# Kernel tuning notes

Hardware: AMD Instinct MI355X
Metric: run time of the kernel (lower is better)

The kernel has to match this reference:

```python
import jax, jax.numpy as jnp
import numpy as np

DIM, HID, E, K = 512, 2048, 8, 2

def setup_inputs() -> dict:
    key = jax.random.key(0)
    ks = jax.random.split(key, 6)
    x = jax.random.normal(ks[0], (8, 4096, DIM), dtype=jnp.float32)
    assign = jax.random.randint(ks[1], (8, 4096, K), 0, E, dtype=jnp.int32)
    W1 = jax.random.normal(ks[2], (E, DIM, HID), dtype=jnp.float32) * 0.02
    b1 = jnp.zeros((E, HID), dtype=jnp.float32)
    W2 = jax.random.normal(ks[3], (E, HID, DIM), dtype=jnp.float32) * 0.02
    b2 = jnp.zeros((E, DIM), dtype=jnp.float32)
    return {"x": x, "assign": assign, "W1": W1, "b1": b1, "W2": W2, "b2": b2}

def reference(x, assign, W1, b1, W2, b2):
    # x: [B,S,D]; assign: [B,S,K] expert ids; hash router => uniform weights 1/K
    B, S, D = x.shape
    k = assign.shape[-1]
    num_experts = W1.shape[0]
    flat_x = x.reshape(B * S, D)
    flat_assign = assign.reshape(B * S, k)
    inv_k = jnp.asarray(1.0 / k, dtype=x.dtype)
    out = jnp.zeros((B * S, D), dtype=x.dtype)
    for e in range(num_experts):  # small fixed expert count
        # total routing weight for this expert per token (handles duplicate slots)
        token_w = (flat_assign == e).sum(-1).astype(x.dtype) * inv_k  # [B*S]
        h = jax.nn.relu(flat_x @ W1[e] + b1[e])        # [B*S, hidden]
        y = h @ W2[e] + b2[e]                          # [B*S, D]
        out = out + y * token_w[:, None]               # zero weight => zero contribution
    return out.reshape(B, S, D)
```

## Files before the change

### kernel.cpp

```cpp
#include <hip/hip_runtime.h>


#define NTOK 32768
#define DIM  512
#define HID  2048
#define NE   8
#define TM   64
#define MAXTILE 128

#define XBASE 0
#define HBASE 65536
#define RBASE 98304
#define LDS_BYTES 163840

typedef __attribute__((ext_vector_type(8))) short short8;
typedef __attribute__((ext_vector_type(4))) float f32x4;
typedef __attribute__((ext_vector_type(4))) unsigned short us4b;
typedef unsigned short ushort_t;

__device__ __forceinline__ unsigned short f2bf(float f) {
  union { float f; unsigned u; } v; v.f = f;
  unsigned r = v.u + 0x7FFFu + ((v.u >> 16) & 1u);
  return (unsigned short)(r >> 16);
}
__device__ __forceinline__ float bf2f(unsigned short s) {
  union { unsigned u; float f; } v; v.u = ((unsigned)s) << 16;
  return v.f;
}
__device__ __forceinline__ void g2l16(const void* g, void* l) {
  __builtin_amdgcn_global_load_lds(
      (const __attribute__((address_space(1))) void*)g,
      (__attribute__((address_space(3))) void*)l, 16, 0, 0);
}

#define SCHB __builtin_amdgcn_sched_barrier(0)
#define VMW4 do { asm volatile("s_waitcnt vmcnt(4)" ::: "memory"); SCHB; } while (0)
#define MFMA16(a, b, c) __builtin_amdgcn_mfma_f32_16x16x32_bf16(a, b, c, 0, 0, 0)

__device__ __forceinline__ void transp_body(const float* __restrict__ src,
                                            ushort_t* __restrict__ dst,
                                            int R, int C, int rb, int cb,
                                            int t, float tile[64][68]) {
  {
    const int tr = t >> 2, tc = (t & 3) * 16;
    const f32x4* s = (const f32x4*)(src + (size_t)(rb + tr) * C + cb + tc);
    f32x4 v0 = __builtin_nontemporal_load(s + 0);
    f32x4 v1 = __builtin_nontemporal_load(s + 1);
    f32x4 v2 = __builtin_nontemporal_load(s + 2);
    f32x4 v3 = __builtin_nontemporal_load(s + 3);
    *(f32x4*)&tile[tr][tc + 0]  = v0;
    *(f32x4*)&tile[tr][tc + 4]  = v1;
    *(f32x4*)&tile[tr][tc + 8]  = v2;
    *(f32x4*)&tile[tr][tc + 12] = v3;
  }
  __syncthreads();
  {
    const int n = t >> 2, ks = (t & 3) * 16;
    short8 o0, o1;
#pragma unroll
    for (int j = 0; j < 8; ++j) o0[j] = (short)f2bf(tile[ks + j][n]);
#pragma unroll
    for (int j = 0; j < 8; ++j) o1[j] = (short)f2bf(tile[ks + 8 + j][n]);
    ushort_t* d = dst + (size_t)(cb + n) * R + rb + ks;
    *(short8*)(d) = o0;
    *(short8*)(d + 8) = o1;
  }
}

__global__ __launch_bounds__(256) void moe_prep(
    const float* __restrict__ W1, const float* __restrict__ W2,
    ushort_t* __restrict__ W1b, ushort_t* __restrict__ W2b,
    const int* __restrict__ assign, int* __restrict__ cnt,
    int* __restrict__ lists) {
  __shared__ float tile[64][68];
  __shared__ int lcnt[NE], gbase[NE];
  const int b = blockIdx.x;
  const int t = threadIdx.x;
  if (b < 2048) {
    int e = b >> 8, rem = b & 255;
    int rb = (rem >> 5) * 64, cb = (rem & 31) * 64;
    transp_body(W1 + (size_t)e * DIM * HID, W1b + (size_t)e * HID * DIM,
                DIM, HID, rb, cb, t, tile);
  } else if (b < 4096) {
    int bb = b - 2048;
    int e = bb >> 8, rem = bb & 255;
    int rb = (rem >> 3) * 64, cb = (rem & 7) * 64;
    transp_body(W2 + (size_t)e * HID * DIM, W2b + (size_t)e * DIM * HID,
                HID, DIM, rb, cb, t, tile);
  } else {
    int tt = (b - 4096) * 256 + t;
    if (t < NE) lcnt[t] = 0;
    __syncthreads();
    int a0 = assign[2 * tt + 0];
    int a1 = assign[2 * tt + 1];
    int r0, r1 = -1;
    r0 = atomicAdd(&lcnt[a0], 1);
    if (a0 != a1) r1 = atomicAdd(&lcnt[a1], 1);
    __syncthreads();
    if (t < NE) gbase[t] = atomicAdd(&cnt[t], lcnt[t]);
    __syncthreads();
    if (a0 == a1) {
      lists[a0 * NTOK + gbase[a0] + r0] = tt | 0x10000;
    } else {
      lists[a0 * NTOK + gbase[a0] + r0] = tt;
      lists[a1 * NTOK + gbase[a1] + r1] = tt | (1 << 17);
    }
  }
}

__global__ __launch_bounds__(256) void moe_combine(
    const ushort_t* __restrict__ Yb, float* __restrict__ out) {
  size_t i = ((size_t)blockIdx.x * 256 + threadIdx.x) * 8;
  short8 y0 = *(const short8*)(Yb + i);
  short8 y1 = *(const short8*)(Yb + (size_t)NTOK * DIM + i);
  f32x4 o0, o1;
#pragma unroll
  for (int j = 0; j < 4; ++j)
    o0[j] = 0.5f * (bf2f((unsigned short)y0[j]) + bf2f((unsigned short)y1[j]));
#pragma unroll
  for (int j = 0; j < 4; ++j)
    o1[j] = 0.5f * (bf2f((unsigned short)y0[4 + j]) + bf2f((unsigned short)y1[4 + j]));
  *(f32x4*)(out + i) = o0;
  *(f32x4*)(out + i + 4) = o1;
}

__global__ __launch_bounds__(512, 1) void moe_gemm(
    const float* __restrict__ x, const ushort_t* __restrict__ W1b,
    const float* __restrict__ b1, const ushort_t* __restrict__ W2b,
    const float* __restrict__ b2, const int* __restrict__ cnt,
    const int* __restrict__ lists, ushort_t* __restrict__ Yb) {
  extern __shared__ char smem[];

  const int id = blockIdx.x;
  const int e = id & 7;
  const int tile = id >> 3;
  const int n_e = cnt[e];
  const int t0 = tile * TM;
  if (t0 >= n_e) return;

  const int tid = threadIdx.x;
  const int wid = tid >> 6;
  const int lane = tid & 63;
  const int lr = lane & 15, lg = lane >> 4;
  const int lr7 = lr & 7;
  const int lrq = (lr >> 1) & 3;
  const int l3 = lane >> 3, l7 = lane & 7;

  char* const ring0 = smem + RBASE + wid * 8192;

  const ushort_t* gW1c = W1b + ((size_t)(e * HID) + wid * 32 + l3) * DIM + (l7 ^ l3) * 8;
  const ushort_t* gW2c = W2b + ((size_t)(e * DIM) + wid * 64 + (lane >> 2)) * HID +
                         ((lane & 3) ^ ((lane >> 3) & 3)) * 8;
  const float* b1e = b1 + (size_t)e * HID + wid * 32 + lg * 4;

  auto IS_G1 = [&](const ushort_t* wb, int p, int half, int slot) {
    char* d = ring0 + slot * 2048 + lane * 16;
    const ushort_t* g = wb + (size_t)(half * 16) * DIM + p * 64;
    g2l16(g, d);
    g2l16(g + (size_t)8 * DIM, d + 1024);
  };
  auto IS_G2 = [&](const ushort_t* wb, int q, int h, int slot) {
    char* d = ring0 + slot * 2048 + lane * 16;
    const ushort_t* g = wb + (size_t)(h * 32) * HID + q * 32;
    g2l16(g, d);
    g2l16(g + (size_t)16 * HID, d + 1024);
  };

#define B1LOAD(d0, d1, BI) do { \
  const float* a_ = b1e + (BI) * 256; \
  asm volatile("global_load_dwordx4 %0, %2, off\n\t" \
               "global_load_dwordx4 %1, %2, off offset:64" \
               : "=&v"(d0), "=&v"(d1) : "v"(a_)); \
} while (0)

#define XRD(dst, nf, p, kf) do { \
  const int row_ = (nf) * 16 + lr; \
  const int u_ = (p) * 8 + (kf) * 4 + lg; \
  dst = *(const short8*)(smem + XBASE + row_ * 1024 + \
        ((u_ & ~7) | ((u_ & 7) ^ (row_ & 7))) * 16); } while (0)
#define HRD(dst, nf, q) do { \
  const int row_ = (nf) * 16 + lr; \
  const int u_ = (q) * 4 + lg; \
  dst = *(const short8*)(smem + HBASE + row_ * 512 + \
        ((u_ & ~7) | ((u_ & 7) ^ (row_ & 7))) * 16); } while (0)
#define W1RD(dst, S, kf) \
  dst = *(const short8*)(ring0 + (S) * 2048 + lr * 128 + ((((kf) * 4 + lg) ^ lr7) * 16))
#define W2RD(dst, S, half) \
  dst = *(const short8*)(ring0 + (S) * 2048 + ((half) * 16 + lr) * 64 + ((lg ^ lrq) * 16))

#define G1_PHASE(p, S0, S1, ISS) do { \
  VMW4; \
  short8 wa0k0, wa1k0, wa0k1, wa1k1; \
  W1RD(wa0k0, S0, 0); W1RD(wa1k0, S1, 0); W1RD(wa0k1, S0, 1); W1RD(wa1k1, S1, 1); \
  SCHB; \
  short8 x00, x01, x02, x03, x10, x11, x12, x13; \
  XRD(x00, 0, p, 0); XRD(x01, 1, p, 0); XRD(x02, 2, p, 0); XRD(x03, 3, p, 0); \
  XRD(x10, 0, p, 1); XRD(x11, 1, p, 1); XRD(x12, 2, p, 1); XRD(x13, 3, p, 1); \
  SCHB; \
  asm volatile("s_waitcnt lgkmcnt(8)" ::: "memory"); SCHB; \
  ISS; SCHB; \
  __builtin_amdgcn_s_setprio(1); \
  acc1[0][0] = MFMA16(wa0k0, x00, acc1[0][0]); acc1[1][0] = MFMA16(wa1k0, x00, acc1[1][0]); \
  acc1[0][1] = MFMA16(wa0k0, x01, acc1[0][1]); acc1[1][1] = MFMA16(wa1k0, x01, acc1[1][1]); \
  acc1[0][2] = MFMA16(wa0k0, x02, acc1[0][2]); acc1[1][2] = MFMA16(wa1k0, x02, acc1[1][2]); \
  acc1[0][3] = MFMA16(wa0k0, x03, acc1[0][3]); acc1[1][3] = MFMA16(wa1k0, x03, acc1[1][3]); \
  acc1[0][0] = MFMA16(wa0k1, x10, acc1[0][0]); acc1[1][0] = MFMA16(wa1k1, x10, acc1[1][0]); \
  acc1[0][1] = MFMA16(wa0k1, x11, acc1[0][1]); acc1[1][1] = MFMA16(wa1k1, x11, acc1[1][1]); \
  acc1[0][2] = MFMA16(wa0k1, x12, acc1[0][2]); acc1[1][2] = MFMA16(wa1k1, x12, acc1[1][2]); \
  acc1[0][3] = MFMA16(wa0k1, x13, acc1[0][3]); acc1[1][3] = MFMA16(wa1k1, x13, acc1[1][3]); \
  __builtin_amdgcn_s_setprio(0); SCHB; \
} while (0)

#define G2_PHASE(q, S0, S1, ISS) do { \
  VMW4; \
  short8 w0, w1, w2, w3; \
  W2RD(w0, S0, 0); W2RD(w1, S0, 1); W2RD(w2, S1, 0); W2RD(w3, S1, 1); \
  SCHB; \
  short8 h0, h1, h2, h3; \
  HRD(h0, 0, q); HRD(h1, 1, q); HRD(h2, 2, q); HRD(h3, 3, q); \
  SCHB; \
  asm volatile("s_waitcnt lgkmcnt(4)" ::: "memory"); SCHB; \
  ISS; SCHB; \
  __builtin_amdgcn_s_setprio(1); \
  acc2[0][0] = MFMA16(w0, h0, acc2[0][0]); acc2[0][1] = MFMA16(w0, h1, acc2[0][1]); \
  acc2[0][2] = MFMA16(w0, h2, acc2[0][2]); acc2[0][3] = MFMA16(w0, h3, acc2[0][3]); \
  acc2[1][0] = MFMA16(w1, h0, acc2[1][0]); acc2[1][1] = MFMA16(w1, h1, acc2[1][1]); \
  acc2[1][2] = MFMA16(w1, h2, acc2[1][2]); acc2[1][3] = MFMA16(w1, h3, acc2[1][3]); \
  acc2[2][0] = MFMA16(w2, h0, acc2[2][0]); acc2[2][1] = MFMA16(w2, h1, acc2[2][1]); \
  acc2[2][2] = MFMA16(w2, h2, acc2[2][2]); acc2[2][3] = MFMA16(w2, h3, acc2[2][3]); \
  acc2[3][0] = MFMA16(w3, h0, acc2[3][0]); acc2[3][1] = MFMA16(w3, h1, acc2[3][1]); \
  acc2[3][2] = MFMA16(w3, h2, acc2[3][2]); acc2[3][3] = MFMA16(w3, h3, acc2[3][3]); \
  __builtin_amdgcn_s_setprio(0); SCHB; \
} while (0)

#define HWRITE(Q0, Q1) do { \
  _Pragma("unroll") \
  for (int mf_ = 0; mf_ < 2; ++mf_) { \
    f32x4 bq_ = mf_ ? (Q1) : (Q0); \
    int hl_ = wid * 32 + mf_ * 16 + lg * 4; \
    int u_ = hl_ >> 3; \
    _Pragma("unroll") \
    for (int nf_ = 0; nf_ < 4; ++nf_) { \
      int tokr_ = nf_ * 16 + lr; \
      us4b pk_; \
      pk_.x = f2bf(fmaxf(acc1[mf_][nf_][0] + bq_[0], 0.0f)); \
      pk_.y = f2bf(fmaxf(acc1[mf_][nf_][1] + bq_[1], 0.0f)); \
      pk_.z = f2bf(fmaxf(acc1[mf_][nf_][2] + bq_[2], 0.0f)); \
      pk_.w = f2bf(fmaxf(acc1[mf_][nf_][3] + bq_[3], 0.0f)); \
      int u2_ = (u_ & ~7) | ((u_ & 7) ^ (tokr_ & 7)); \
      *(us4b*)(smem + HBASE + tokr_ * 512 + u2_ * 16 + (lg & 1) * 8) = pk_; \
    } \
  } \
} while (0)

#define CHUNK(C, BU0, BU1, BN0, BN1) do { \
  f32x4 acc1[2][4]; \
  _Pragma("unroll") \
  for (int i_ = 0; i_ < 2; ++i_) \
    _Pragma("unroll") \
    for (int j_ = 0; j_ < 4; ++j_) acc1[i_][j_] = f32x4{0.f, 0.f, 0.f, 0.f}; \
  G1_PHASE(0, 0, 1, { B1LOAD(BN0, BN1, ((C) < 7 ? (C) + 1 : 7)); \
                      IS_G1(gW1c, 2, 0, 0); IS_G1(gW1c, 2, 1, 1); }); \
  G1_PHASE(1, 2, 3, { IS_G1(gW1c, 3, 0, 2); IS_G1(gW1c, 3, 1, 3); }); \
  G1_PHASE(2, 0, 1, { IS_G1(gW1c, 4, 0, 0); IS_G1(gW1c, 4, 1, 1); }); \
  G1_PHASE(3, 2, 3, { IS_G1(gW1c, 5, 0, 2); IS_G1(gW1c, 5, 1, 3); }); \
  G1_PHASE(4, 0, 1, { IS_G1(gW1c, 6, 0, 0); IS_G1(gW1c, 6, 1, 1); }); \
  G1_PHASE(5, 2, 3, { IS_G1(gW1c, 7, 0, 2); IS_G1(gW1c, 7, 1, 3); }); \
  G1_PHASE(6, 0, 1, { IS_G2(gW2c, 0, 0, 0); IS_G2(gW2c, 0, 1, 1); }); \
  G1_PHASE(7, 2, 3, { IS_G2(gW2c, 1, 0, 2); IS_G2(gW2c, 1, 1, 3); }); \
  asm volatile("s_waitcnt lgkmcnt(0)" ::: "memory"); \
  __builtin_amdgcn_s_barrier(); SCHB; \
  HWRITE(BU0, BU1); \
  SCHB; \
  asm volatile("s_waitcnt lgkmcnt(0)" ::: "memory"); \
  __builtin_amdgcn_s_barrier(); SCHB; \
  G2_PHASE(0, 0, 1, { IS_G2(gW2c, 2, 0, 0); IS_G2(gW2c, 2, 1, 1); }); \
  G2_PHASE(1, 2, 3, { IS_G2(gW2c, 3, 0, 2); IS_G2(gW2c, 3, 1, 3); }); \
  G2_PHASE(2, 0, 1, { IS_G2(gW2c, 4, 0, 0); IS_G2(gW2c, 4, 1, 1); }); \
  G2_PHASE(3, 2, 3, { IS_G2(gW2c, 5, 0, 2); IS_G2(gW2c, 5, 1, 3); }); \
  G2_PHASE(4, 0, 1, { IS_G2(gW2c, 6, 0, 0); IS_G2(gW2c, 6, 1, 1); }); \
  G2_PHASE(5, 2, 3, { IS_G2(gW2c, 7, 0, 2); IS_G2(gW2c, 7, 1, 3); }); \
  G2_PHASE(6, 0, 1, { IS_G1(gW1c + 131072, 0, 0, 0); IS_G1(gW1c + 131072, 0, 1, 1); }); \
  G2_PHASE(7, 2, 3, { IS_G1(gW1c + 131072, 1, 0, 2); IS_G1(gW1c + 131072, 1, 1, 3); }); \
  gW1c += 131072; gW2c += 256; \
} while (0)

  {
    int row = tid >> 3;
    int idx = t0 + row;
    int tok = lists[e * NTOK + (idx < n_e ? idx : 0)] & 0xFFFF;
    const float* xr = x + (size_t)tok * DIM;
#pragma unroll
    for (int i = 0; i < 8; ++i) {
      int u = (tid & 7) + 8 * i;
      f32x4 v0 = __builtin_nontemporal_load((const f32x4*)(xr + u * 8));
      f32x4 v1 = __builtin_nontemporal_load((const f32x4*)(xr + u * 8 + 4));
      short8 pk;
      pk[0] = (short)f2bf(v0.x); pk[1] = (short)f2bf(v0.y);
      pk[2] = (short)f2bf(v0.z); pk[3] = (short)f2bf(v0.w);
      pk[4] = (short)f2bf(v1.x); pk[5] = (short)f2bf(v1.y);
      pk[6] = (short)f2bf(v1.z); pk[7] = (short)f2bf(v1.w);
      int su = (u & ~7) | ((u & 7) ^ (row & 7));
      *(short8*)(smem + XBASE + row * 1024 + su * 16) = pk;
    }
  }
  __syncthreads();

  f32x4 b1A0, b1A1, b1B0, b1B1;
  B1LOAD(b1A0, b1A1, 0);
  IS_G1(gW1c, 0, 0, 0); IS_G1(gW1c, 0, 1, 1);
  IS_G1(gW1c, 1, 0, 2); IS_G1(gW1c, 1, 1, 3);
  SCHB;

  f32x4 acc2[4][4];
#pragma unroll
  for (int i = 0; i < 4; ++i)
#pragma unroll
    for (int j = 0; j < 4; ++j) acc2[i][j] = f32x4{0.f, 0.f, 0.f, 0.f};

#pragma unroll 1
  for (int cc = 0; cc < 4; ++cc) {
    const int c0 = cc * 2;
    CHUNK(c0,     b1A0, b1A1, b1B0, b1B1);
    CHUNK(c0 + 1, b1B0, b1B1, b1A0, b1A1);
  }
  asm volatile("s_waitcnt vmcnt(0)" ::: "memory");
  SCHB;
  asm volatile("" :: "v"(b1A0), "v"(b1A1));

  f32x4 b2q[4];
#pragma unroll
  for (int mf = 0; mf < 4; ++mf)
    b2q[mf] = *(const f32x4*)(b2 + e * DIM + wid * 64 + mf * 16 + lg * 4);

#pragma unroll
  for (int nf = 0; nf < 4; ++nf) {
    int gi = t0 + nf * 16 + lr;
    if (gi >= n_e) continue;
    int ent = lists[e * NTOK + gi];
    int tok = ent & 0xFFFF;
    int slot = (ent >> 17) & 1;
    size_t base = ((size_t)(slot * NTOK + tok)) * DIM + wid * 64 + lg * 4;
#pragma unroll
    for (int mf = 0; mf < 4; ++mf) {
      f32x4 y = acc2[mf][nf] + b2q[mf];
      us4b pk;
      pk.x = f2bf(y[0]); pk.y = f2bf(y[1]); pk.z = f2bf(y[2]); pk.w = f2bf(y[3]);
      *(us4b*)(Yb + base + mf * 16) = pk;
      if (ent & 0x10000)
        *(us4b*)(Yb + base + (size_t)NTOK * DIM + mf * 16) = pk;
    }
  }
}

extern "C" void kernel_launch(void* const* d_in, const int* in_sizes, int n_in,
                              void* d_out, int out_size, void* d_ws, size_t ws_size,
                              hipStream_t stream) {
  const float* x      = (const float*)d_in[0];
  const int*   assign = (const int*)d_in[1];
  const float* W1     = (const float*)d_in[2];
  const float* b1     = (const float*)d_in[3];
  const float* W2     = (const float*)d_in[4];
  const float* b2     = (const float*)d_in[5];
  float* out = (float*)d_out;

  char* ws = (char*)d_ws;
  int* cnt   = (int*)ws;
  int* lists = (int*)(ws + 1024);
  ushort_t* W1b = (ushort_t*)(ws + (2ull << 20));
  ushort_t* W2b = (ushort_t*)(ws + (2ull << 20) + 18874368ull);
  ushort_t* Yb  = (ushort_t*)(ws + (2ull << 20) + 2ull * 18874368ull);

  (void)hipMemsetAsync(cnt, 0, 256, stream);

  moe_prep<<<4096 + NTOK / 256, 256, 0, stream>>>(W1, W2, W1b, W2b,
                                                  assign, cnt, lists);

  (void)hipFuncSetAttribute((const void*)moe_gemm,
                            hipFuncAttributeMaxDynamicSharedMemorySize, LDS_BYTES);
  moe_gemm<<<NE * MAXTILE, 512, LDS_BYTES, stream>>>(x, W1b, b1, W2b, b2,
                                                     cnt, lists, Yb);

  moe_combine<<<NTOK * DIM / 2048, 256, 0, stream>>>(Yb, out);
}
```

Baseline: 355.4 us.

## Restructure fused MoE FFN into 512-wide hidden chunks with 64-row weight tiles

Replaces the eight 256-hidden chunks with four 512-hidden chunks. Each wave now computes a 64x64 GEMM1 tile (acc1 grows to 4x4) and stages four 8-row weight groups per slot in a two-slot ring of 4KB slots. In exchange, the H buffer is handed off twice per chunk, each with its own barrier and bias load. The intent is more MFMA per LDS weight read and fewer loop iterations, at the cost of higher register pressure from the larger accumulators and extra handoff barriers.

```diff
diff --git a/kernel.cpp b/kernel.cpp
--- a/kernel.cpp
+++ b/kernel.cpp
@@ -143,146 +143,91 @@
   const int lane = tid & 63;
   const int lr = lane & 15, lg = lane >> 4;
   const int lr7 = lr & 7;
-  const int lrq = (lr >> 1) & 3;
-  const int l3 = lane >> 3, l7 = lane & 7;
-
-  char* const ring0 = smem + RBASE + wid * 8192;
-
-  const ushort_t* gW1c = W1b + ((size_t)(e * HID) + wid * 32 + l3) * DIM + (l7 ^ l3) * 8;
-  const ushort_t* gW2c = W2b + ((size_t)(e * DIM) + wid * 64 + (lane >> 2)) * HID +
-                         ((lane & 3) ^ ((lane >> 3) & 3)) * 8;
-  const float* b1e = b1 + (size_t)e * HID + wid * 32 + lg * 4;
-
-  auto IS_G1 = [&](const ushort_t* wb, int p, int half, int slot) {
-    char* d = ring0 + slot * 2048 + lane * 16;
-    const ushort_t* g = wb + (size_t)(half * 16) * DIM + p * 64;
+  const int lsub = lane >> 3;
+  const int unit = (lane & 7) ^ lsub;
+  const int etahi = unit >> 2;
+  const int kq = unit & 3;
+
+  char* const ringw = smem + RBASE + wid * 8192;
+
+  const ushort_t* gW1w = W1b +
+      ((size_t)(e * HID + wid * 32 + etahi * 256 + lsub)) * DIM + kq * 8;
+  const ushort_t* gW2w = W2b +
+      ((size_t)(e * DIM + wid * 64 + etahi * 32 + lsub)) * HID + kq * 8;
+
+  auto stW1 = [&](int c, int p, int sl) {
+    const ushort_t* g = gW1w + (size_t)c * (512 * DIM) + p * 32;
+    char* d = ringw + sl * 4096 + lane * 16;
     g2l16(g, d);
-    g2l16(g + (size_t)8 * DIM, d + 1024);
+    g2l16(g + 1 * 8 * DIM, d + 1024);
+    g2l16(g + 2 * 8 * DIM, d + 2048);
+    g2l16(g + 3 * 8 * DIM, d + 3072);
   };
-  auto IS_G2 = [&](const ushort_t* wb, int q, int h, int slot) {
-    char* d = ring0 + slot * 2048 + lane * 16;
-    const ushort_t* g = wb + (size_t)(h * 32) * HID + q * 32;
+  auto stW2 = [&](int c, int h, int q, int sl) {
+    const ushort_t* g = gW2w + c * 512 + h * 256 + q * 32;
+    char* d = ringw + sl * 4096 + lane * 16;
     g2l16(g, d);
-    g2l16(g + (size_t)16 * HID, d + 1024);
+    g2l16(g + 1 * 8 * HID, d + 1024);
+    g2l16(g + 2 * 8 * HID, d + 2048);
+    g2l16(g + 3 * 8 * HID, d + 3072);
   };
 
-#define B1LOAD(d0, d1, BI) do { \
-  const float* a_ = b1e + (BI) * 256; \
-  asm volatile("global_load_dwordx4 %0, %2, off\n\t" \
-               "global_load_dwordx4 %1, %2, off offset:64" \
-               : "=&v"(d0), "=&v"(d1) : "v"(a_)); \
-} while (0)
-
-#define XRD(dst, nf, p, kf) do { \
-  const int row_ = (nf) * 16 + lr; \
-  const int u_ = (p) * 8 + (kf) * 4 + lg; \
-  dst = *(const short8*)(smem + XBASE + row_ * 1024 + \
-        ((u_ & ~7) | ((u_ & 7) ^ (row_ & 7))) * 16); } while (0)
-#define HRD(dst, nf, q) do { \
-  const int row_ = (nf) * 16 + lr; \
-  const int u_ = (q) * 4 + lg; \
-  dst = *(const short8*)(smem + HBASE + row_ * 512 + \
-        ((u_ & ~7) | ((u_ & 7) ^ (row_ & 7))) * 16); } while (0)
-#define W1RD(dst, S, kf) \
-  dst = *(const short8*)(ring0 + (S) * 2048 + lr * 128 + ((((kf) * 4 + lg) ^ lr7) * 16))
-#define W2RD(dst, S, half) \
-  dst = *(const short8*)(ring0 + (S) * 2048 + ((half) * 16 + lr) * 64 + ((lg ^ lrq) * 16))
-
-#define G1_PHASE(p, S0, S1, ISS) do { \
-  VMW4; \
-  short8 wa0k0, wa1k0, wa0k1, wa1k1; \
-  W1RD(wa0k0, S0, 0); W1RD(wa1k0, S1, 0); W1RD(wa0k1, S0, 1); W1RD(wa1k1, S1, 1); \
-  SCHB; \
-  short8 x00, x01, x02, x03, x10, x11, x12, x13; \
-  XRD(x00, 0, p, 0); XRD(x01, 1, p, 0); XRD(x02, 2, p, 0); XRD(x03, 3, p, 0); \
-  XRD(x10, 0, p, 1); XRD(x11, 1, p, 1); XRD(x12, 2, p, 1); XRD(x13, 3, p, 1); \
-  SCHB; \
-  asm volatile("s_waitcnt lgkmcnt(8)" ::: "memory"); SCHB; \
-  ISS; SCHB; \
-  __builtin_amdgcn_s_setprio(1); \
-  acc1[0][0] = MFMA16(wa0k0, x00, acc1[0][0]); acc1[1][0] = MFMA16(wa1k0, x00, acc1[1][0]); \
-  acc1[0][1] = MFMA16(wa0k0, x01, acc1[0][1]); acc1[1][1] = MFMA16(wa1k0, x01, acc1[1][1]); \
-  acc1[0][2] = MFMA16(wa0k0, x02, acc1[0][2]); acc1[1][2] = MFMA16(wa1k0, x02, acc1[1][2]); \
-  acc1[0][3] = MFMA16(wa0k0, x03, acc1[0][3]); acc1[1][3] = MFMA16(wa1k0, x03, acc1[1][3]); \
-  acc1[0][0] = MFMA16(wa0k1, x10, acc1[0][0]); acc1[1][0] = MFMA16(wa1k1, x10, acc1[1][0]); \
-  acc1[0][1] = MFMA16(wa0k1, x11, acc1[0][1]); acc1[1][1] = MFMA16(wa1k1, x11, acc1[1][1]); \
-  acc1[0][2] = MFMA16(wa0k1, x12, acc1[0][2]); acc1[1][2] = MFMA16(wa1k1, x12, acc1[1][2]); \
-  acc1[0][3] = MFMA16(wa0k1, x13, acc1[0][3]); acc1[1][3] = MFMA16(wa1k1, x13, acc1[1][3]); \
+#define RD_W(dst, mf, SL) \
+  dst = *(const short8*)(ringw + (SL) * 4096 + (((mf) & 1) * 16 + lr) * 128 + \
+                         (((((mf) >> 1) * 4 + lg) ^ lr7) * 16))
+
+#define G1P(p, SL, ISSUE) do { \
+  ISSUE; SCHB; VMW4; \
+  short8 wf[4], xf[4]; \
+  _Pragma("unroll") for (int mf = 0; mf < 4; ++mf) RD_W(wf[mf], mf, SL); \
+  _Pragma("unroll") for (int nf = 0; nf < 4; ++nf) { \
+    int u_ = (p) * 4 + lg; int row_ = nf * 16 + lr; \
+    xf[nf] = *(const short8*)(smem + XBASE + row_ * 1024 + \
+             ((u_ & ~7) | ((u_ & 7) ^ lr7)) * 16); } \
+  SCHB; __builtin_amdgcn_s_setprio(1); \
+  _Pragma("unroll") for (int mf = 0; mf < 4; ++mf) \
+    _Pragma("unroll") for (int nf = 0; nf < 4; ++nf) \
+      acc1[mf][nf] = MFMA16(wf[mf], xf[nf], acc1[mf][nf]); \
   __builtin_amdgcn_s_setprio(0); SCHB; \
 } while (0)
 
-#define G2_PHASE(q, S0, S1, ISS) do { \
-  VMW4; \
-  short8 w0, w1, w2, w3; \
-  W2RD(w0, S0, 0); W2RD(w1, S0, 1); W2RD(w2, S1, 0); W2RD(w3, S1, 1); \
-  SCHB; \
-  short8 h0, h1, h2, h3; \
-  HRD(h0, 0, q); HRD(h1, 1, q); HRD(h2, 2, q); HRD(h3, 3, q); \
-  SCHB; \
-  asm volatile("s_waitcnt lgkmcnt(4)" ::: "memory"); SCHB; \
-  ISS; SCHB; \
-  __builtin_amdgcn_s_setprio(1); \
-  acc2[0][0] = MFMA16(w0, h0, acc2[0][0]); acc2[0][1] = MFMA16(w0, h1, acc2[0][1]); \
-  acc2[0][2] = MFMA16(w0, h2, acc2[0][2]); acc2[0][3] = MFMA16(w0, h3, acc2[0][3]); \
-  acc2[1][0] = MFMA16(w1, h0, acc2[1][0]); acc2[1][1] = MFMA16(w1, h1, acc2[1][1]); \
-  acc2[1][2] = MFMA16(w1, h2, acc2[1][2]); acc2[1][3] = MFMA16(w1, h3, acc2[1][3]); \
-  acc2[2][0] = MFMA16(w2, h0, acc2[2][0]); acc2[2][1] = MFMA16(w2, h1, acc2[2][1]); \
-  acc2[2][2] = MFMA16(w2, h2, acc2[2][2]); acc2[2][3] = MFMA16(w2, h3, acc2[2][3]); \
-  acc2[3][0] = MFMA16(w3, h0, acc2[3][0]); acc2[3][1] = MFMA16(w3, h1, acc2[3][1]); \
-  acc2[3][2] = MFMA16(w3, h2, acc2[3][2]); acc2[3][3] = MFMA16(w3, h3, acc2[3][3]); \
+#define G2P(q, SL, ISSUE) do { \
+  ISSUE; SCHB; VMW4; \
+  short8 wf[4], hf[4]; \
+  _Pragma("unroll") for (int mf = 0; mf < 4; ++mf) RD_W(wf[mf], mf, SL); \
+  _Pragma("unroll") for (int nf = 0; nf < 4; ++nf) { \
+    int u_ = (q) * 4 + lg; int row_ = nf * 16 + lr; \
+    hf[nf] = *(const short8*)(smem + HBASE + row_ * 512 + \
+             ((u_ & ~7) | ((u_ & 7) ^ lr7)) * 16); } \
+  SCHB; __builtin_amdgcn_s_setprio(1); \
+  _Pragma("unroll") for (int mf = 0; mf < 4; ++mf) \
+    _Pragma("unroll") for (int nf = 0; nf < 4; ++nf) \
+      acc2[mf][nf] = MFMA16(wf[mf], hf[nf], acc2[mf][nf]); \
   __builtin_amdgcn_s_setprio(0); SCHB; \
 } while (0)
 
-#define HWRITE(Q0, Q1) do { \
-  _Pragma("unroll") \
-  for (int mf_ = 0; mf_ < 2; ++mf_) { \
-    f32x4 bq_ = mf_ ? (Q1) : (Q0); \
-    int hl_ = wid * 32 + mf_ * 16 + lg * 4; \
-    int u_ = hl_ >> 3; \
-    _Pragma("unroll") \
-    for (int nf_ = 0; nf_ < 4; ++nf_) { \
-      int tokr_ = nf_ * 16 + lr; \
-      us4b pk_; \
-      pk_.x = f2bf(fmaxf(acc1[mf_][nf_][0] + bq_[0], 0.0f)); \
-      pk_.y = f2bf(fmaxf(acc1[mf_][nf_][1] + bq_[1], 0.0f)); \
-      pk_.z = f2bf(fmaxf(acc1[mf_][nf_][2] + bq_[2], 0.0f)); \
-      pk_.w = f2bf(fmaxf(acc1[mf_][nf_][3] + bq_[3], 0.0f)); \
-      int u2_ = (u_ & ~7) | ((u_ & 7) ^ (tokr_ & 7)); \
-      *(us4b*)(smem + HBASE + tokr_ * 512 + u2_ * 16 + (lg & 1) * 8) = pk_; \
-    } \
-  } \
-} while (0)
-
-#define CHUNK(C, BU0, BU1, BN0, BN1) do { \
-  f32x4 acc1[2][4]; \
-  _Pragma("unroll") \
-  for (int i_ = 0; i_ < 2; ++i_) \
-    _Pragma("unroll") \
-    for (int j_ = 0; j_ < 4; ++j_) acc1[i_][j_] = f32x4{0.f, 0.f, 0.f, 0.f}; \
-  G1_PHASE(0, 0, 1, { B1LOAD(BN0, BN1, ((C) < 7 ? (C) + 1 : 7)); \
-                      IS_G1(gW1c, 2, 0, 0); IS_G1(gW1c, 2, 1, 1); }); \
-  G1_PHASE(1, 2, 3, { IS_G1(gW1c, 3, 0, 2); IS_G1(gW1c, 3, 1, 3); }); \
-  G1_PHASE(2, 0, 1, { IS_G1(gW1c, 4, 0, 0); IS_G1(gW1c, 4, 1, 1); }); \
-  G1_PHASE(3, 2, 3, { IS_G1(gW1c, 5, 0, 2); IS_G1(gW1c, 5, 1, 3); }); \
-  G1_PHASE(4, 0, 1, { IS_G1(gW1c, 6, 0, 0); IS_G1(gW1c, 6, 1, 1); }); \
-  G1_PHASE(5, 2, 3, { IS_G1(gW1c, 7, 0, 2); IS_G1(gW1c, 7, 1, 3); }); \
-  G1_PHASE(6, 0, 1, { IS_G2(gW2c, 0, 0, 0); IS_G2(gW2c, 0, 1, 1); }); \
-  G1_PHASE(7, 2, 3, { IS_G2(gW2c, 1, 0, 2); IS_G2(gW2c, 1, 1, 3); }); \
+#define HANDOFF(h) do { \
   asm volatile("s_waitcnt lgkmcnt(0)" ::: "memory"); \
   __builtin_amdgcn_s_barrier(); SCHB; \
-  HWRITE(BU0, BU1); \
+  { const float* b1p = b1 + (size_t)e * HID + c * 512 + (h) * 256 + \
+                       wid * 32 + lg * 4; \
+    f32x4 bq0 = *(const f32x4*)(b1p); \
+    f32x4 bq1 = *(const f32x4*)(b1p + 16); \
+    _Pragma("unroll") for (int m2 = 0; m2 < 2; ++m2) { \
+      int hl = wid * 32 + m2 * 16 + lg * 4; int u = hl >> 3; \
+      _Pragma("unroll") for (int nf = 0; nf < 4; ++nf) { \
+        int tokr = nf * 16 + lr; \
+        us4b pk; \
+        pk.x = f2bf(fmaxf(acc1[(h)*2+m2][nf][0] + (m2 ? bq1[0] : bq0[0]), 0.f)); \
+        pk.y = f2bf(fmaxf(acc1[(h)*2+m2][nf][1] + (m2 ? bq1[1] : bq0[1]), 0.f)); \
+        pk.z = f2bf(fmaxf(acc1[(h)*2+m2][nf][2] + (m2 ? bq1[2] : bq0[2]), 0.f)); \
+        pk.w = f2bf(fmaxf(acc1[(h)*2+m2][nf][3] + (m2 ? bq1[3] : bq0[3]), 0.f)); \
+        *(us4b*)(smem + HBASE + tokr * 512 + \
+                 ((u & ~7) | ((u & 7) ^ (tokr & 7))) * 16 + (lg & 1) * 8) = pk; \
+      } } } \
   SCHB; \
   asm volatile("s_waitcnt lgkmcnt(0)" ::: "memory"); \
   __builtin_amdgcn_s_barrier(); SCHB; \
-  G2_PHASE(0, 0, 1, { IS_G2(gW2c, 2, 0, 0); IS_G2(gW2c, 2, 1, 1); }); \
-  G2_PHASE(1, 2, 3, { IS_G2(gW2c, 3, 0, 2); IS_G2(gW2c, 3, 1, 3); }); \
-  G2_PHASE(2, 0, 1, { IS_G2(gW2c, 4, 0, 0); IS_G2(gW2c, 4, 1, 1); }); \
-  G2_PHASE(3, 2, 3, { IS_G2(gW2c, 5, 0, 2); IS_G2(gW2c, 5, 1, 3); }); \
-  G2_PHASE(4, 0, 1, { IS_G2(gW2c, 6, 0, 0); IS_G2(gW2c, 6, 1, 1); }); \
-  G2_PHASE(5, 2, 3, { IS_G2(gW2c, 7, 0, 2); IS_G2(gW2c, 7, 1, 3); }); \
-  G2_PHASE(6, 0, 1, { IS_G1(gW1c + 131072, 0, 0, 0); IS_G1(gW1c + 131072, 0, 1, 1); }); \
-  G2_PHASE(7, 2, 3, { IS_G1(gW1c + 131072, 1, 0, 2); IS_G1(gW1c + 131072, 1, 1, 3); }); \
-  gW1c += 131072; gW2c += 256; \
 } while (0)
 
   {
@@ -306,11 +251,7 @@
   }
   __syncthreads();
 
-  f32x4 b1A0, b1A1, b1B0, b1B1;
-  B1LOAD(b1A0, b1A1, 0);
-  IS_G1(gW1c, 0, 0, 0); IS_G1(gW1c, 0, 1, 1);
-  IS_G1(gW1c, 1, 0, 2); IS_G1(gW1c, 1, 1, 3);
-  SCHB;
+  stW1(0, 0, 0);
 
   f32x4 acc2[4][4];
 #pragma unroll
@@ -319,14 +260,54 @@
     for (int j = 0; j < 4; ++j) acc2[i][j] = f32x4{0.f, 0.f, 0.f, 0.f};
 
 #pragma unroll 1
-  for (int cc = 0; cc < 4; ++cc) {
-    const int c0 = cc * 2;
-    CHUNK(c0,     b1A0, b1A1, b1B0, b1B1);
-    CHUNK(c0 + 1, b1B0, b1B1, b1A0, b1A1);
+  for (int c = 0; c < 4; ++c) {
+    f32x4 acc1[4][4];
+#pragma unroll
+    for (int i = 0; i < 4; ++i)
+#pragma unroll
+      for (int j = 0; j < 4; ++j) acc1[i][j] = f32x4{0.f, 0.f, 0.f, 0.f};
+
+    G1P(0,  0, stW1(c, 1, 1));
+    G1P(1,  1, stW1(c, 2, 0));
+    G1P(2,  0, stW1(c, 3, 1));
+    G1P(3,  1, stW1(c, 4, 0));
+    G1P(4,  0, stW1(c, 5, 1));
+    G1P(5,  1, stW1(c, 6, 0));
+    G1P(6,  0, stW1(c, 7, 1));
+    G1P(7,  1, stW1(c, 8, 0));
+    G1P(8,  0, stW1(c, 9, 1));
+    G1P(9,  1, stW1(c, 10, 0));
+    G1P(10, 0, stW1(c, 11, 1));
+    G1P(11, 1, stW1(c, 12, 0));
+    G1P(12, 0, stW1(c, 13, 1));
+    G1P(13, 1, stW1(c, 14, 0));
+    G1P(14, 0, stW1(c, 15, 1));
+    G1P(15, 1, stW2(c, 0, 0, 0));
+
+    HANDOFF(0);
+
+    G2P(0, 0, stW2(c, 0, 1, 1));
+    G2P(1, 1, stW2(c, 0, 2, 0));
+    G2P(2, 0, stW2(c, 0, 3, 1));
+    G2P(3, 1, stW2(c, 0, 4, 0));
+    G2P(4, 0, stW2(c, 0, 5, 1));
+    G2P(5, 1, stW2(c, 0, 6, 0));
+    G2P(6, 0, stW2(c, 0, 7, 1));
+    G2P(7, 1, stW2(c, 1, 0, 0));
+
+    HANDOFF(1);
+
+    G2P(0, 0, stW2(c, 1, 1, 1));
+    G2P(1, 1, stW2(c, 1, 2, 0));
+    G2P(2, 0, stW2(c, 1, 3, 1));
+    G2P(3, 1, stW2(c, 1, 4, 0));
+    G2P(4, 0, stW2(c, 1, 5, 1));
+    G2P(5, 1, stW2(c, 1, 6, 0));
+    G2P(6, 0, stW2(c, 1, 7, 1));
+    G2P(7, 1, { int cn = (c < 3) ? c + 1 : 0; stW1(cn, 0, 0); });
   }
   asm volatile("s_waitcnt vmcnt(0)" ::: "memory");
   SCHB;
-  asm volatile("" :: "v"(b1A0), "v"(b1A1));
 
   f32x4 b2q[4];
 #pragma unroll
```

After: 378.8 us. 6.6% more time.

## Widen hidden chunk to 512 per block pass with K-step-32 weight staging

Applied to the files above, without the earlier changes.

Restructures the fused MoE FFN loop so each outer chunk covers 512 hidden units (4 chunks instead of 8), with each wave holding a 4x4 accumulator tile in GEMM1 and issuing 16 MFMAs per X fragment read. Weight staging now uses 32-wide K slices with a unified swizzled ring layout for W1 and W2. The H handoff happens twice per chunk. The aim is to raise MFMA-per-LDS-read reuse and halve loop overhead and barriers per hidden unit, at the cost of more accumulator registers, which may lower occupancy or cause spills.

```diff
diff --git a/kernel.cpp b/kernel.cpp
--- a/kernel.cpp
+++ b/kernel.cpp
@@ -143,146 +143,163 @@
   const int lane = tid & 63;
   const int lr = lane & 15, lg = lane >> 4;
   const int lr7 = lr & 7;
-  const int lrq = (lr >> 1) & 3;
-  const int l3 = lane >> 3, l7 = lane & 7;
-
-  char* const ring0 = smem + RBASE + wid * 8192;
-
-  const ushort_t* gW1c = W1b + ((size_t)(e * HID) + wid * 32 + l3) * DIM + (l7 ^ l3) * 8;
-  const ushort_t* gW2c = W2b + ((size_t)(e * DIM) + wid * 64 + (lane >> 2)) * HID +
-                         ((lane & 3) ^ ((lane >> 3) & 3)) * 8;
+  const int lr3 = lr & 3;
+
+  char* const ringw = smem + RBASE + wid * 8192;
+
+  const ushort_t* gW1L = W1b +
+      ((size_t)(e * HID + wid * 32 + (lane >> 2))) * DIM +
+      ((lane & 3) ^ ((lane >> 2) & 3)) * 8;
+  const ushort_t* gW2L = W2b +
+      ((size_t)(e * DIM + wid * 64 + (lane >> 2))) * HID +
+      ((lane & 3) ^ ((lane >> 2) & 3)) * 8;
   const float* b1e = b1 + (size_t)e * HID + wid * 32 + lg * 4;
 
-  auto IS_G1 = [&](const ushort_t* wb, int p, int half, int slot) {
-    char* d = ring0 + slot * 2048 + lane * 16;
-    const ushort_t* g = wb + (size_t)(half * 16) * DIM + p * 64;
-    g2l16(g, d);
-    g2l16(g + (size_t)8 * DIM, d + 1024);
+  auto stW1 = [&](int c, int p, int sA, int sB) {
+    const ushort_t* g = gW1L + (size_t)(c * 512) * DIM + p * 32;
+    char* dA = ringw + sA * 2048 + lane * 16;
+    char* dB = ringw + sB * 2048 + lane * 16;
+    g2l16(g, dA);
+    g2l16(g + (size_t)16 * DIM, dA + 1024);
+    g2l16(g + (size_t)256 * DIM, dB);
+    g2l16(g + (size_t)272 * DIM, dB + 1024);
   };
-  auto IS_G2 = [&](const ushort_t* wb, int q, int h, int slot) {
-    char* d = ring0 + slot * 2048 + lane * 16;
-    const ushort_t* g = wb + (size_t)(h * 32) * HID + q * 32;
-    g2l16(g, d);
-    g2l16(g + (size_t)16 * HID, d + 1024);
+  auto stW2 = [&](int c, int h, int q, int sA, int sB) {
+    const ushort_t* g = gW2L + c * 512 + h * 256 + q * 32;
+    char* dA = ringw + sA * 2048 + lane * 16;
+    char* dB = ringw + sB * 2048 + lane * 16;
+    g2l16(g, dA);
+    g2l16(g + (size_t)16 * HID, dA + 1024);
+    g2l16(g + (size_t)32 * HID, dB);
+    g2l16(g + (size_t)48 * HID, dB + 1024);
   };
 
-#define B1LOAD(d0, d1, BI) do { \
-  const float* a_ = b1e + (BI) * 256; \
-  asm volatile("global_load_dwordx4 %0, %2, off\n\t" \
-               "global_load_dwordx4 %1, %2, off offset:64" \
-               : "=&v"(d0), "=&v"(d1) : "v"(a_)); \
+#define B1LOAD(d0, d1, d2, d3, BI) do { \
+  const float* a_ = b1e + (size_t)(BI) * 512; \
+  asm volatile("global_load_dwordx4 %0, %4, off\n\t" \
+               "global_load_dwordx4 %1, %4, off offset:64\n\t" \
+               "global_load_dwordx4 %2, %4, off offset:1024\n\t" \
+               "global_load_dwordx4 %3, %4, off offset:1088" \
+               : "=&v"(d0), "=&v"(d1), "=&v"(d2), "=&v"(d3) : "v"(a_)); \
 } while (0)
 
-#define XRD(dst, nf, p, kf) do { \
-  const int row_ = (nf) * 16 + lr; \
-  const int u_ = (p) * 8 + (kf) * 4 + lg; \
+#define RD_W(dst, S, m2) \
+  dst = *(const short8*)(ringw + (S) * 2048 + ((m2) * 16 + lr) * 64 + \
+                         ((lg ^ lr3) * 16))
+#define XRD(dst, nf, p) do { \
+  const int u_ = (p) * 4 + lg; const int row_ = (nf) * 16 + lr; \
   dst = *(const short8*)(smem + XBASE + row_ * 1024 + \
-        ((u_ & ~7) | ((u_ & 7) ^ (row_ & 7))) * 16); } while (0)
+        ((u_ & ~7) | ((u_ & 7) ^ lr7)) * 16); } while (0)
 #define HRD(dst, nf, q) do { \
-  const int row_ = (nf) * 16 + lr; \
-  const int u_ = (q) * 4 + lg; \
+  const int u_ = (q) * 4 + lg; const int row_ = (nf) * 16 + lr; \
   dst = *(const short8*)(smem + HBASE + row_ * 512 + \
-        ((u_ & ~7) | ((u_ & 7) ^ (row_ & 7))) * 16); } while (0)
-#define W1RD(dst, S, kf) \
-  dst = *(const short8*)(ring0 + (S) * 2048 + lr * 128 + ((((kf) * 4 + lg) ^ lr7) * 16))
-#define W2RD(dst, S, half) \
-  dst = *(const short8*)(ring0 + (S) * 2048 + ((half) * 16 + lr) * 64 + ((lg ^ lrq) * 16))
-
-#define G1_PHASE(p, S0, S1, ISS) do { \
+        ((u_ & ~7) | ((u_ & 7) ^ lr7)) * 16); } while (0)
+
+#define G1P(p, S0, S1, ISSUE) do { \
   VMW4; \
-  short8 wa0k0, wa1k0, wa0k1, wa1k1; \
-  W1RD(wa0k0, S0, 0); W1RD(wa1k0, S1, 0); W1RD(wa0k1, S0, 1); W1RD(wa1k1, S1, 1); \
+  short8 wf0, wf1, wf2, wf3; \
+  RD_W(wf0, S0, 0); RD_W(wf1, S0, 1); RD_W(wf2, S1, 0); RD_W(wf3, S1, 1); \
   SCHB; \
-  short8 x00, x01, x02, x03, x10, x11, x12, x13; \
-  XRD(x00, 0, p, 0); XRD(x01, 1, p, 0); XRD(x02, 2, p, 0); XRD(x03, 3, p, 0); \
-  XRD(x10, 0, p, 1); XRD(x11, 1, p, 1); XRD(x12, 2, p, 1); XRD(x13, 3, p, 1); \
+  short8 xf0, xf1, xf2, xf3; \
+  XRD(xf0, 0, p); XRD(xf1, 1, p); XRD(xf2, 2, p); XRD(xf3, 3, p); \
   SCHB; \
-  asm volatile("s_waitcnt lgkmcnt(8)" ::: "memory"); SCHB; \
-  ISS; SCHB; \
+  asm volatile("s_waitcnt lgkmcnt(4)" ::: "memory"); SCHB; \
+  ISSUE; SCHB; \
   __builtin_amdgcn_s_setprio(1); \
-  acc1[0][0] = MFMA16(wa0k0, x00, acc1[0][0]); acc1[1][0] = MFMA16(wa1k0, x00, acc1[1][0]); \
-  acc1[0][1] = MFMA16(wa0k0, x01, acc1[0][1]); acc1[1][1] = MFMA16(wa1k0, x01, acc1[1][1]); \
-  acc1[0][2] = MFMA16(wa0k0, x02, acc1[0][2]); acc1[1][2] = MFMA16(wa1k0, x02, acc1[1][2]); \
-  acc1[0][3] = MFMA16(wa0k0, x03, acc1[0][3]); acc1[1][3] = MFMA16(wa1k0, x03, acc1[1][3]); \
-  acc1[0][0] = MFMA16(wa0k1, x10, acc1[0][0]); acc1[1][0] = MFMA16(wa1k1, x10, acc1[1][0]); \
-  acc1[0][1] = MFMA16(wa0k1, x11, acc1[0][1]); acc1[1][1] = MFMA16(wa1k1, x11, acc1[1][1]); \
-  acc1[0][2] = MFMA16(wa0k1, x12, acc1[0][2]); acc1[1][2] = MFMA16(wa1k1, x12, acc1[1][2]); \
-  acc1[0][3] = MFMA16(wa0k1, x13, acc1[0][3]); acc1[1][3] = MFMA16(wa1k1, x13, acc1[1][3]); \
+  acc1[0][0] = MFMA16(wf0, xf0, acc1[0][0]); acc1[0][1] = MFMA16(wf0, xf1, acc1[0][1]); \
+  acc1[0][2] = MFMA16(wf0, xf2, acc1[0][2]); acc1[0][3] = MFMA16(wf0, xf3, acc1[0][3]); \
+  acc1[1][0] = MFMA16(wf1, xf0, acc1[1][0]); acc1[1][1] = MFMA16(wf1, xf1, acc1[1][1]); \
+  acc1[1][2] = MFMA16(wf1, xf2, acc1[1][2]); acc1[1][3] = MFMA16(wf1, xf3, acc1[1][3]); \
+  acc1[2][0] = MFMA16(wf2, xf0, acc1[2][0]); acc1[2][1] = MFMA16(wf2, xf1, acc1[2][1]); \
+  acc1[2][2] = MFMA16(wf2, xf2, acc1[2][2]); acc1[2][3] = MFMA16(wf2, xf3, acc1[2][3]); \
+  acc1[3][0] = MFMA16(wf3, xf0, acc1[3][0]); acc1[3][1] = MFMA16(wf3, xf1, acc1[3][1]); \
+  acc1[3][2] = MFMA16(wf3, xf2, acc1[3][2]); acc1[3][3] = MFMA16(wf3, xf3, acc1[3][3]); \
   __builtin_amdgcn_s_setprio(0); SCHB; \
 } while (0)
 
-#define G2_PHASE(q, S0, S1, ISS) do { \
+#define G2P(q, S0, S1, ISSUE) do { \
   VMW4; \
-  short8 w0, w1, w2, w3; \
-  W2RD(w0, S0, 0); W2RD(w1, S0, 1); W2RD(w2, S1, 0); W2RD(w3, S1, 1); \
+  short8 wf0, wf1, wf2, wf3; \
+  RD_W(wf0, S0, 0); RD_W(wf1, S0, 1); RD_W(wf2, S1, 0); RD_W(wf3, S1, 1); \
   SCHB; \
-  short8 h0, h1, h2, h3; \
-  HRD(h0, 0, q); HRD(h1, 1, q); HRD(h2, 2, q); HRD(h3, 3, q); \
+  short8 hf0, hf1, hf2, hf3; \
+  HRD(hf0, 0, q); HRD(hf1, 1, q); HRD(hf2, 2, q); HRD(hf3, 3, q); \
   SCHB; \
   asm volatile("s_waitcnt lgkmcnt(4)" ::: "memory"); SCHB; \
-  ISS; SCHB; \
+  ISSUE; SCHB; \
   __builtin_amdgcn_s_setprio(1); \
-  acc2[0][0] = MFMA16(w0, h0, acc2[0][0]); acc2[0][1] = MFMA16(w0, h1, acc2[0][1]); \
-  acc2[0][2] = MFMA16(w0, h2, acc2[0][2]); acc2[0][3] = MFMA16(w0, h3, acc2[0][3]); \
-  acc2[1][0] = MFMA16(w1, h0, acc2[1][0]); acc2[1][1] = MFMA16(w1, h1, acc2[1][1]); \
-  acc2[1][2] = MFMA16(w1, h2, acc2[1][2]); acc2[1][3] = MFMA16(w1, h3, acc2[1][3]); \
-  acc2[2][0] = MFMA16(w2, h0, acc2[2][0]); acc2[2][1] = MFMA16(w2, h1, acc2[2][1]); \
-  acc2[2][2] = MFMA16(w2, h2, acc2[2][2]); acc2[2][3] = MFMA16(w2, h3, acc2[2][3]); \
-  acc2[3][0] = MFMA16(w3, h0, acc2[3][0]); acc2[3][1] = MFMA16(w3, h1, acc2[3][1]); \
-  acc2[3][2] = MFMA16(w3, h2, acc2[3][2]); acc2[3][3] = MFMA16(w3, h3, acc2[3][3]); \
+  acc2[0][0] = MFMA16(wf0, hf0, acc2[0][0]); acc2[0][1] = MFMA16(wf0, hf1, acc2[0][1]); \
+  acc2[0][2] = MFMA16(wf0, hf2, acc2[0][2]); acc2[0][3] = MFMA16(wf0, hf3, acc2[0][3]); \
+  acc2[1][0] = MFMA16(wf1, hf0, acc2[1][0]); acc2[1][1] = MFMA16(wf1, hf1, acc2[1][1]); \
+  acc2[1][2] = MFMA16(wf1, hf2, acc2[1][2]); acc2[1][3] = MFMA16(wf1, hf3, acc2[1][3]); \
+  acc2[2][0] = MFMA16(wf2, hf0, acc2[2][0]); acc2[2][1] = MFMA16(wf2, hf1, acc2[2][1]); \
+  acc2[2][2] = MFMA16(wf2, hf2, acc2[2][2]); acc2[2][3] = MFMA16(wf2, hf3, acc2[2][3]); \
+  acc2[3][0] = MFMA16(wf3, hf0, acc2[3][0]); acc2[3][1] = MFMA16(wf3, hf1, acc2[3][1]); \
+  acc2[3][2] = MFMA16(wf3, hf2, acc2[3][2]); acc2[3][3] = MFMA16(wf3, hf3, acc2[3][3]); \
   __builtin_amdgcn_s_setprio(0); SCHB; \
 } while (0)
 
-#define HWRITE(Q0, Q1) do { \
-  _Pragma("unroll") \
-  for (int mf_ = 0; mf_ < 2; ++mf_) { \
-    f32x4 bq_ = mf_ ? (Q1) : (Q0); \
-    int hl_ = wid * 32 + mf_ * 16 + lg * 4; \
-    int u_ = hl_ >> 3; \
-    _Pragma("unroll") \
-    for (int nf_ = 0; nf_ < 4; ++nf_) { \
-      int tokr_ = nf_ * 16 + lr; \
-      us4b pk_; \
-      pk_.x = f2bf(fmaxf(acc1[mf_][nf_][0] + bq_[0], 0.0f)); \
-      pk_.y = f2bf(fmaxf(acc1[mf_][nf_][1] + bq_[1], 0.0f)); \
-      pk_.z = f2bf(fmaxf(acc1[mf_][nf_][2] + bq_[2], 0.0f)); \
-      pk_.w = f2bf(fmaxf(acc1[mf_][nf_][3] + bq_[3], 0.0f)); \
-      int u2_ = (u_ & ~7) | ((u_ & 7) ^ (tokr_ & 7)); \
-      *(us4b*)(smem + HBASE + tokr_ * 512 + u2_ * 16 + (lg & 1) * 8) = pk_; \
-    } \
-  } \
-} while (0)
-
-#define CHUNK(C, BU0, BU1, BN0, BN1) do { \
-  f32x4 acc1[2][4]; \
-  _Pragma("unroll") \
-  for (int i_ = 0; i_ < 2; ++i_) \
-    _Pragma("unroll") \
-    for (int j_ = 0; j_ < 4; ++j_) acc1[i_][j_] = f32x4{0.f, 0.f, 0.f, 0.f}; \
-  G1_PHASE(0, 0, 1, { B1LOAD(BN0, BN1, ((C) < 7 ? (C) + 1 : 7)); \
-                      IS_G1(gW1c, 2, 0, 0); IS_G1(gW1c, 2, 1, 1); }); \
-  G1_PHASE(1, 2, 3, { IS_G1(gW1c, 3, 0, 2); IS_G1(gW1c, 3, 1, 3); }); \
-  G1_PHASE(2, 0, 1, { IS_G1(gW1c, 4, 0, 0); IS_G1(gW1c, 4, 1, 1); }); \
-  G1_PHASE(3, 2, 3, { IS_G1(gW1c, 5, 0, 2); IS_G1(gW1c, 5, 1, 3); }); \
-  G1_PHASE(4, 0, 1, { IS_G1(gW1c, 6, 0, 0); IS_G1(gW1c, 6, 1, 1); }); \
-  G1_PHASE(5, 2, 3, { IS_G1(gW1c, 7, 0, 2); IS_G1(gW1c, 7, 1, 3); }); \
-  G1_PHASE(6, 0, 1, { IS_G2(gW2c, 0, 0, 0); IS_G2(gW2c, 0, 1, 1); }); \
-  G1_PHASE(7, 2, 3, { IS_G2(gW2c, 1, 0, 2); IS_G2(gW2c, 1, 1, 3); }); \
+#define HANDOFF(h, Q0, Q1) do { \
   asm volatile("s_waitcnt lgkmcnt(0)" ::: "memory"); \
   __builtin_amdgcn_s_barrier(); SCHB; \
-  HWRITE(BU0, BU1); \
+  _Pragma("unroll") for (int m2 = 0; m2 < 2; ++m2) { \
+    f32x4 bq_ = m2 ? (Q1) : (Q0); \
+    int hl_ = wid * 32 + m2 * 16 + lg * 4; int u_ = hl_ >> 3; \
+    _Pragma("unroll") for (int nf = 0; nf < 4; ++nf) { \
+      int tokr_ = nf * 16 + lr; \
+      us4b pk_; \
+      pk_.x = f2bf(fmaxf(acc1[(h) * 2 + m2][nf][0] + bq_[0], 0.f)); \
+      pk_.y = f2bf(fmaxf(acc1[(h) * 2 + m2][nf][1] + bq_[1], 0.f)); \
+      pk_.z = f2bf(fmaxf(acc1[(h) * 2 + m2][nf][2] + bq_[2], 0.f)); \
+      pk_.w = f2bf(fmaxf(acc1[(h) * 2 + m2][nf][3] + bq_[3], 0.f)); \
+      *(us4b*)(smem + HBASE + tokr_ * 512 + \
+               ((u_ & ~7) | ((u_ & 7) ^ (tokr_ & 7))) * 16 + (lg & 1) * 8) = pk_; \
+    } } \
   SCHB; \
   asm volatile("s_waitcnt lgkmcnt(0)" ::: "memory"); \
   __builtin_amdgcn_s_barrier(); SCHB; \
-  G2_PHASE(0, 0, 1, { IS_G2(gW2c, 2, 0, 0); IS_G2(gW2c, 2, 1, 1); }); \
-  G2_PHASE(1, 2, 3, { IS_G2(gW2c, 3, 0, 2); IS_G2(gW2c, 3, 1, 3); }); \
-  G2_PHASE(2, 0, 1, { IS_G2(gW2c, 4, 0, 0); IS_G2(gW2c, 4, 1, 1); }); \
-  G2_PHASE(3, 2, 3, { IS_G2(gW2c, 5, 0, 2); IS_G2(gW2c, 5, 1, 3); }); \
-  G2_PHASE(4, 0, 1, { IS_G2(gW2c, 6, 0, 0); IS_G2(gW2c, 6, 1, 1); }); \
-  G2_PHASE(5, 2, 3, { IS_G2(gW2c, 7, 0, 2); IS_G2(gW2c, 7, 1, 3); }); \
-  G2_PHASE(6, 0, 1, { IS_G1(gW1c + 131072, 0, 0, 0); IS_G1(gW1c + 131072, 0, 1, 1); }); \
-  G2_PHASE(7, 2, 3, { IS_G1(gW1c + 131072, 1, 0, 2); IS_G1(gW1c + 131072, 1, 1, 3); }); \
-  gW1c += 131072; gW2c += 256; \
+} while (0)
+
+#define CHUNK(C, BU0, BU1, BU2, BU3, BN0, BN1, BN2, BN3) do { \
+  f32x4 acc1[4][4]; \
+  _Pragma("unroll") for (int i_ = 0; i_ < 4; ++i_) \
+    _Pragma("unroll") for (int j_ = 0; j_ < 4; ++j_) \
+      acc1[i_][j_] = f32x4{0.f, 0.f, 0.f, 0.f}; \
+  G1P(0,  0, 1, { B1LOAD(BN0, BN1, BN2, BN3, ((C) + 1) & 3); \
+                  stW1((C), 2, 0, 1); }); \
+  G1P(1,  2, 3, stW1((C), 3, 2, 3)); \
+  G1P(2,  0, 1, stW1((C), 4, 0, 1)); \
+  G1P(3,  2, 3, stW1((C), 5, 2, 3)); \
+  G1P(4,  0, 1, stW1((C), 6, 0, 1)); \
+  G1P(5,  2, 3, stW1((C), 7, 2, 3)); \
+  G1P(6,  0, 1, stW1((C), 8, 0, 1)); \
+  G1P(7,  2, 3, stW1((C), 9, 2, 3)); \
+  G1P(8,  0, 1, stW1((C), 10, 0, 1)); \
+  G1P(9,  2, 3, stW1((C), 11, 2, 3)); \
+  G1P(10, 0, 1, stW1((C), 12, 0, 1)); \
+  G1P(11, 2, 3, stW1((C), 13, 2, 3)); \
+  G1P(12, 0, 1, stW1((C), 14, 0, 1)); \
+  G1P(13, 2, 3, stW1((C), 15, 2, 3)); \
+  G1P(14, 0, 1, stW2((C), 0, 0, 0, 1)); \
+  G1P(15, 2, 3, stW2((C), 0, 1, 2, 3)); \
+  HANDOFF(0, BU0, BU1); \
+  G2P(0, 0, 1, stW2((C), 0, 2, 0, 1)); \
+  G2P(1, 2, 3, stW2((C), 0, 3, 2, 3)); \
+  G2P(2, 0, 1, stW2((C), 0, 4, 0, 1)); \
+  G2P(3, 2, 3, stW2((C), 0, 5, 2, 3)); \
+  G2P(4, 0, 1, stW2((C), 0, 6, 0, 1)); \
+  G2P(5, 2, 3, stW2((C), 0, 7, 2, 3)); \
+  G2P(6, 0, 1, stW2((C), 1, 0, 0, 1)); \
+  G2P(7, 2, 3, stW2((C), 1, 1, 2, 3)); \
+  HANDOFF(1, BU2, BU3); \
+  G2P(0, 0, 1, stW2((C), 1, 2, 0, 1)); \
+  G2P(1, 2, 3, stW2((C), 1, 3, 2, 3)); \
+  G2P(2, 0, 1, stW2((C), 1, 4, 0, 1)); \
+  G2P(3, 2, 3, stW2((C), 1, 5, 2, 3)); \
+  G2P(4, 0, 1, stW2((C), 1, 6, 0, 1)); \
+  G2P(5, 2, 3, stW2((C), 1, 7, 2, 3)); \
+  G2P(6, 0, 1, stW1(((C) + 1) & 3, 0, 0, 1)); \
+  G2P(7, 2, 3, stW1(((C) + 1) & 3, 1, 2, 3)); \
 } while (0)
 
   {
@@ -306,10 +323,10 @@
   }
   __syncthreads();
 
-  f32x4 b1A0, b1A1, b1B0, b1B1;
-  B1LOAD(b1A0, b1A1, 0);
-  IS_G1(gW1c, 0, 0, 0); IS_G1(gW1c, 0, 1, 1);
-  IS_G1(gW1c, 1, 0, 2); IS_G1(gW1c, 1, 1, 3);
+  f32x4 bA0, bA1, bA2, bA3, bB0, bB1, bB2, bB3;
+  B1LOAD(bA0, bA1, bA2, bA3, 0);
+  stW1(0, 0, 0, 1);
+  stW1(0, 1, 2, 3);
   SCHB;
 
   f32x4 acc2[4][4];
@@ -319,14 +336,14 @@
     for (int j = 0; j < 4; ++j) acc2[i][j] = f32x4{0.f, 0.f, 0.f, 0.f};
 
 #pragma unroll 1
-  for (int cc = 0; cc < 4; ++cc) {
+  for (int cc = 0; cc < 2; ++cc) {
     const int c0 = cc * 2;
-    CHUNK(c0,     b1A0, b1A1, b1B0, b1B1);
-    CHUNK(c0 + 1, b1B0, b1B1, b1A0, b1A1);
+    CHUNK(c0,     bA0, bA1, bA2, bA3, bB0, bB1, bB2, bB3);
+    CHUNK(c0 + 1, bB0, bB1, bB2, bB3, bA0, bA1, bA2, bA3);
   }
   asm volatile("s_waitcnt vmcnt(0)" ::: "memory");
   SCHB;
-  asm volatile("" :: "v"(b1A0), "v"(b1A1));
+  asm volatile("" :: "v"(bA0), "v"(bA1), "v"(bA2), "v"(bA3));
 
   f32x4 b2q[4];
 #pragma unroll
```

Result: slower. 371.4 us (+4.5%).
